# Kernel optimization log

Hardware: AMD Instinct MI355X
Metric: run time of the kernel (lower is better)

## Reference

```python
import jax, jax.numpy as jnp
import numpy as np

N_PER_DEG = 30000
MAX_DEG = 6
MIN_DEG = 0
N_ATOMS = N_PER_DEG * (MAX_DEG + 1)  # 210000, atoms sorted by degree
N_FEAT = 128
NB_FILTER = 128
NB_AFFINE = 2 * MAX_DEG + (1 - MIN_DEG)  # 13


def setup_inputs() -> dict:
    key = jax.random.key(0)
    ks = jax.random.split(key, 2 + MAX_DEG)
    atoms = jax.random.normal(ks[0], (N_ATOMS, N_FEAT), dtype=jnp.float32)
    # glorot-ish scale for the 13 affine weights
    W = jax.random.normal(ks[1], (NB_AFFINE, N_FEAT, NB_FILTER), dtype=jnp.float32) * (1.0 / np.sqrt(N_FEAT))
    b = jnp.zeros((NB_AFFINE, NB_FILTER), dtype=jnp.float32)
    # deg_slice[d] = (start, count) for degree d in 0..MAX_DEG; equal-size buckets
    deg_slice = jnp.asarray(
        np.stack([np.arange(MAX_DEG + 1) * N_PER_DEG,
                  np.full(MAX_DEG + 1, N_PER_DEG)], axis=1).astype(np.int32))
    inp = {"atoms": atoms, "W": W, "b": b, "deg_slice": deg_slice}
    for d in range(1, MAX_DEG + 1):
        inp[f"adj{d}"] = jax.random.randint(ks[1 + d], (N_PER_DEG, d), 0, N_ATOMS, dtype=jnp.int32)
    return inp


def reference(atoms, W, b, deg_slice, adj1, adj2, adj3, adj4, adj5, adj6):
    """Degree-bucketed graph convolution (deepchem GraphConv, linear activation).

    W ordering matches the original iterator: for deg=1..MAX_DEG the pair
    (rel=W[2*(deg-1)], self=W[2*(deg-1)+1]), then deg-0 self uses W[2*MAX_DEG].
    Output concat order: deg 0 bucket first, then deg 1..MAX_DEG.
    """
    adjs = [adj1, adj2, adj3, adj4, adj5, adj6]
    ds = np.asarray(deg_slice)  # structural constant: static slice bounds
    outs = [None] * (MAX_DEG + 1 - MIN_DEG)
    # deg 0: self-affine only
    s0, c0 = int(ds[0, 0]), int(ds[0, 1])
    outs[0] = atoms[s0:s0 + c0] @ W[2 * MAX_DEG] + b[2 * MAX_DEG]
    for deg in range(1, MAX_DEG + 1):
        s, c = int(ds[deg, 0]), int(ds[deg, 1])
        # gather neighbors of each degree-deg atom and sum: (c, deg, F) -> (c, F)
        rel = jnp.take(atoms, adjs[deg - 1], axis=0).sum(axis=1)
        out = (rel @ W[2 * (deg - 1)] + b[2 * (deg - 1)]
               + atoms[s:s + c] @ W[2 * (deg - 1) + 1] + b[2 * (deg - 1) + 1])
        outs[deg] = out
    return jnp.concatenate(outs, axis=0)  # (N_ATOMS, NB_FILTER)
```

## Files before the change

### kernel.cpp

```cpp
#include <hip/hip_runtime.h>
#include <hip/hip_bf16.h>

#define NPD 30000
#define NF  128
#define MAXDEG 6
#define TM  64
#define LDK 136

typedef __attribute__((ext_vector_type(8))) short short8;
typedef __attribute__((ext_vector_type(4))) float floatx4;

__device__ __forceinline__ unsigned short f2bf(float f) {
    __hip_bfloat16 h = __float2bfloat16(f);
    return __builtin_bit_cast(unsigned short, h);
}

__global__ void wt_kernel(const float* __restrict__ W,
                          unsigned short* __restrict__ Wt) {
    __shared__ unsigned short t[32][33];
    const int a  = blockIdx.z;
    const int k0 = blockIdx.x * 32, n0 = blockIdx.y * 32;
    const int tx = threadIdx.x & 31, ty = threadIdx.x >> 5;
    const float*    Wp  = W  + (size_t)a * NF * NF;
    unsigned short* Wtp = Wt + (size_t)a * NF * NF;
#pragma unroll
    for (int i = 0; i < 32; i += 8)
        t[ty + i][tx] = f2bf(Wp[(size_t)(k0 + ty + i) * NF + (n0 + tx)]);
    __syncthreads();
#pragma unroll
    for (int i = 0; i < 32; i += 8)
        Wtp[(size_t)(n0 + ty + i) * NF + (k0 + tx)] = t[tx][ty + i];
}

template <int DEG>
__device__ __forceinline__ void gather_sum(const int* __restrict__ adj,
                                           const float* __restrict__ atoms,
                                           int row_glob, int kc, float* a32) {
    const int* arow = adj + (size_t)row_glob * DEG;
    int idxs[DEG];
#pragma unroll
    for (int j = 0; j < DEG; j++) idxs[j] = arow[j];
#pragma unroll
    for (int i = 0; i < 32; i++) a32[i] = 0.f;
#pragma unroll
    for (int j = 0; j < DEG; j++) {
        const float4* p = (const float4*)(atoms + (size_t)idxs[j] * NF + kc);
#pragma unroll
        for (int q = 0; q < 8; q++) {
            float4 v = p[q];
            a32[q * 4 + 0] += v.x; a32[q * 4 + 1] += v.y;
            a32[q * 4 + 2] += v.z; a32[q * 4 + 3] += v.w;
        }
    }
}

__global__ __launch_bounds__(256) void gconv_kernel(
    const float* __restrict__ atoms,
    const float* __restrict__ W,
    const unsigned short* __restrict__ Wt,
    const float* __restrict__ bvec,
    const int* __restrict__ adj1, const int* __restrict__ adj2,
    const int* __restrict__ adj3, const int* __restrict__ adj4,
    const int* __restrict__ adj5, const int* __restrict__ adj6,
    const int use_wt,
    float* __restrict__ out)
{
    __shared__ unsigned short sA[TM * LDK];

    const int tid  = threadIdx.x;
    const int lane = tid & 63;
    const int wave = tid >> 6;
    const int wr   = wave >> 1, wc = wave & 1;
    const int deg  = blockIdx.y;
    const int row0_local = blockIdx.x * TM;
    const int valid = min(TM, NPD - row0_local);
    const int row0g = deg * NPD + row0_local;

    floatx4 acc[2][4];
#pragma unroll
    for (int i = 0; i < 2; i++)
#pragma unroll
        for (int j = 0; j < 4; j++) acc[i][j] = (floatx4){0.f, 0.f, 0.f, 0.f};

    const int nb = lane & 15;
    const int kq = (lane >> 4) * 8;

    auto run_phase = [&](int wi) {
        const unsigned short* Wtp = Wt + (size_t)wi * NF * NF;
        const float*          Wfp = W  + (size_t)wi * NF * NF;
#pragma unroll
        for (int kk = 0; kk < 4; ++kk) {
            short8 bfr[4];
            if (use_wt) {
#pragma unroll
                for (int nt = 0; nt < 4; ++nt)
                    bfr[nt] = *(const short8*)(Wtp + (size_t)(wc * 64 + nt * 16 + nb) * NF
                                               + kk * 32 + kq);
            } else {
#pragma unroll
                for (int nt = 0; nt < 4; ++nt) {
                    short8 f;
#pragma unroll
                    for (int j = 0; j < 8; ++j)
                        f[j] = (short)f2bf(Wfp[(size_t)(kk * 32 + kq + j) * NF
                                               + (wc * 64 + nt * 16 + nb)]);
                    bfr[nt] = f;
                }
            }
            short8 af[2];
#pragma unroll
            for (int mt = 0; mt < 2; ++mt)
                af[mt] = *(const short8*)(&sA[(wr * 32 + mt * 16 + nb) * LDK + kk * 32 + kq]);
#pragma unroll
            for (int mt = 0; mt < 2; ++mt)
#pragma unroll
                for (int nt = 0; nt < 4; ++nt)
                    acc[mt][nt] = __builtin_amdgcn_mfma_f32_16x16x32_bf16(
                        af[mt], bfr[nt], acc[mt][nt], 0, 0, 0);
        }
    };

    const int rS  = tid >> 2;
    const int kcS = (tid & 3) << 5;
    const int rrS = min(rS, valid - 1);

    {
        const float4* p = (const float4*)(atoms + (size_t)(row0g + rrS) * NF + kcS);
        unsigned ww[16];
#pragma unroll
        for (int q = 0; q < 8; q++) {
            float4 v = p[q];
            ww[q * 2 + 0] = (unsigned)f2bf(v.x) | ((unsigned)f2bf(v.y) << 16);
            ww[q * 2 + 1] = (unsigned)f2bf(v.z) | ((unsigned)f2bf(v.w) << 16);
        }
#pragma unroll
        for (int s = 0; s < 4; s++)
            *(uint4*)(&sA[rS * LDK + kcS + s * 8]) = *(uint4*)&ww[s * 4];
    }
    const int wi_self = (deg == 0) ? 12 : (2 * deg - 1);
    __syncthreads();
    run_phase(wi_self);

    if (deg > 0) {
        __syncthreads();
        float a32[32];
        const int rg = row0_local + rrS;
        switch (deg) {
            case 1: gather_sum<1>(adj1, atoms, rg, kcS, a32); break;
            case 2: gather_sum<2>(adj2, atoms, rg, kcS, a32); break;
            case 3: gather_sum<3>(adj3, atoms, rg, kcS, a32); break;
            case 4: gather_sum<4>(adj4, atoms, rg, kcS, a32); break;
            case 5: gather_sum<5>(adj5, atoms, rg, kcS, a32); break;
            default: gather_sum<6>(adj6, atoms, rg, kcS, a32); break;
        }
        unsigned ww[16];
#pragma unroll
        for (int i = 0; i < 16; i++)
            ww[i] = (unsigned)f2bf(a32[2 * i]) | ((unsigned)f2bf(a32[2 * i + 1]) << 16);
#pragma unroll
        for (int s = 0; s < 4; s++)
            *(uint4*)(&sA[rS * LDK + kcS + s * 8]) = *(uint4*)&ww[s * 4];
        __syncthreads();
        run_phase(2 * (deg - 1));
    }

    float bias[4];
#pragma unroll
    for (int nt = 0; nt < 4; nt++) {
        int n = wc * 64 + nt * 16 + nb;
        float bv = bvec[wi_self * NF + n];
        if (deg > 0) bv += bvec[(2 * (deg - 1)) * NF + n];
        bias[nt] = bv;
    }
    const int rq = (lane >> 4) << 2;
#pragma unroll
    for (int mt = 0; mt < 2; mt++) {
        int rb = wr * 32 + mt * 16 + rq;
#pragma unroll
        for (int reg = 0; reg < 4; reg++) {
            int r = rb + reg;
            if (r < valid) {
                float* op = out + (size_t)(row0g + r) * NF;
#pragma unroll
                for (int nt = 0; nt < 4; nt++) {
                    int n = wc * 64 + nt * 16 + nb;
                    op[n] = acc[mt][nt][reg] + bias[nt];
                }
            }
        }
    }
}

extern "C" void kernel_launch(void* const* d_in, const int* in_sizes, int n_in,
                              void* d_out, int out_size, void* d_ws, size_t ws_size,
                              hipStream_t stream) {
    const float* atoms = (const float*)d_in[0];
    const float* W     = (const float*)d_in[1];
    const float* b     = (const float*)d_in[2];
    const int* adj1 = (const int*)d_in[4];
    const int* adj2 = (const int*)d_in[5];
    const int* adj3 = (const int*)d_in[6];
    const int* adj4 = (const int*)d_in[7];
    const int* adj5 = (const int*)d_in[8];
    const int* adj6 = (const int*)d_in[9];

    const size_t wt_bytes = (size_t)13 * NF * NF * sizeof(unsigned short);
    const int use_wt = (ws_size >= wt_bytes) ? 1 : 0;
    unsigned short* Wt = (unsigned short*)d_ws;

    if (use_wt)
        wt_kernel<<<dim3(4, 4, 13), 256, 0, stream>>>(W, Wt);
    gconv_kernel<<<dim3((NPD + TM - 1) / TM, MAXDEG + 1), 256, 0, stream>>>(
        atoms, W, Wt, b, adj1, adj2, adj3, adj4, adj5, adj6, use_wt,
        (float*)d_out);
}
```

Baseline: 291.8 us.

## Drop LDS staging; each wave loads A fragments directly and owns 32 columns

```diff
diff --git a/kernel.cpp b/kernel.cpp
--- a/kernel.cpp
+++ b/kernel.cpp
@@ -5,7 +5,6 @@
 #define NF  128
 #define MAXDEG 6
 #define TM  64
-#define LDK 136
 
 typedef __attribute__((ext_vector_type(8))) short short8;
 typedef __attribute__((ext_vector_type(4))) float floatx4;
@@ -13,6 +12,14 @@
 __device__ __forceinline__ unsigned short f2bf(float f) {
     __hip_bfloat16 h = __float2bfloat16(f);
     return __builtin_bit_cast(unsigned short, h);
+}
+__device__ __forceinline__ short8 pack8(float4 a, float4 b) {
+    short8 r;
+    r[0] = (short)f2bf(a.x); r[1] = (short)f2bf(a.y);
+    r[2] = (short)f2bf(a.z); r[3] = (short)f2bf(a.w);
+    r[4] = (short)f2bf(b.x); r[5] = (short)f2bf(b.y);
+    r[6] = (short)f2bf(b.z); r[7] = (short)f2bf(b.w);
+    return r;
 }
 
 __global__ void wt_kernel(const float* __restrict__ W,
@@ -32,162 +39,148 @@
         Wtp[(size_t)(n0 + ty + i) * NF + (k0 + tx)] = t[tx][ty + i];
 }
 
+__device__ __forceinline__ void load_bfrags(short8 b[4][2],
+                                            const float* __restrict__ Wf,
+                                            const unsigned short* __restrict__ Wt,
+                                            int use_wt, int wi, int col0, int nb, int kq) {
+    if (use_wt) {
+        const unsigned short* Wp = Wt + (size_t)wi * NF * NF;
+#pragma unroll
+        for (int kk = 0; kk < 4; ++kk)
+#pragma unroll
+            for (int nt = 0; nt < 2; ++nt)
+                b[kk][nt] = *(const short8*)(Wp + (size_t)(col0 + nt * 16 + nb) * NF
+                                             + kk * 32 + kq);
+    } else {
+        const float* Wp = Wf + (size_t)wi * NF * NF;
+#pragma unroll
+        for (int kk = 0; kk < 4; ++kk)
+#pragma unroll
+            for (int nt = 0; nt < 2; ++nt) {
+                short8 f;
+#pragma unroll
+                for (int j = 0; j < 8; ++j)
+                    f[j] = (short)f2bf(Wp[(size_t)(kk * 32 + kq + j) * NF
+                                          + (col0 + nt * 16 + nb)]);
+                b[kk][nt] = f;
+            }
+    }
+}
+
 template <int DEG>
-__device__ __forceinline__ void gather_sum(const int* __restrict__ adj,
-                                           const float* __restrict__ atoms,
-                                           int row_glob, int kc, float* a32) {
-    const int* arow = adj + (size_t)row_glob * DEG;
-    int idxs[DEG];
-#pragma unroll
-    for (int j = 0; j < DEG; j++) idxs[j] = arow[j];
-#pragma unroll
-    for (int i = 0; i < 32; i++) a32[i] = 0.f;
-#pragma unroll
-    for (int j = 0; j < DEG; j++) {
-        const float4* p = (const float4*)(atoms + (size_t)idxs[j] * NF + kc);
-#pragma unroll
-        for (int q = 0; q < 8; q++) {
-            float4 v = p[q];
-            a32[q * 4 + 0] += v.x; a32[q * 4 + 1] += v.y;
-            a32[q * 4 + 2] += v.z; a32[q * 4 + 3] += v.w;
+__device__ __forceinline__ void wave_work(
+    const float* __restrict__ atoms, const float* __restrict__ W,
+    const unsigned short* __restrict__ Wt, const float* __restrict__ bvec,
+    const int* __restrict__ adj, int use_wt,
+    float* __restrict__ out, int row0, int lane, int wave)
+{
+    const int nb   = lane & 15;
+    const int kq   = (lane >> 4) * 8;
+    const int col0 = wave * 32;
+    const int wi_self = (DEG == 0) ? 12 : (2 * DEG - 1);
+    const int wi_rel  = (DEG > 0) ? 2 * (DEG - 1) : 0;
+
+    floatx4 acc[4][2];
+#pragma unroll
+    for (int i = 0; i < 4; i++)
+#pragma unroll
+        for (int j = 0; j < 2; j++) acc[i][j] = (floatx4){0.f, 0.f, 0.f, 0.f};
+
+    {
+        short8 bS[4][2];
+        load_bfrags(bS, W, Wt, use_wt, wi_self, col0, nb, kq);
+#pragma unroll
+        for (int mt = 0; mt < 4; ++mt) {
+            const int rl = min(row0 + mt * 16 + nb, NPD - 1);
+            const float* row = atoms + (size_t)(DEG * NPD + rl) * NF;
+#pragma unroll
+            for (int kk = 0; kk < 4; ++kk) {
+                const float4* p = (const float4*)(row + kk * 32 + kq);
+                float4 v0 = p[0], v1 = p[1];
+                short8 a = pack8(v0, v1);
+#pragma unroll
+                for (int nt = 0; nt < 2; ++nt)
+                    acc[mt][nt] = __builtin_amdgcn_mfma_f32_16x16x32_bf16(
+                        a, bS[kk][nt], acc[mt][nt], 0, 0, 0);
+            }
         }
     }
+
+    if constexpr (DEG > 0) {
+        short8 bR[4][2];
+        load_bfrags(bR, W, Wt, use_wt, wi_rel, col0, nb, kq);
+#pragma unroll
+        for (int mt = 0; mt < 4; ++mt) {
+            const int rl = min(row0 + mt * 16 + nb, NPD - 1);
+            const int* ar = adj + (size_t)rl * DEG;
+            int idxs[DEG];
+#pragma unroll
+            for (int j = 0; j < DEG; ++j) idxs[j] = ar[j];
+#pragma unroll
+            for (int kk = 0; kk < 4; ++kk) {
+                float s[8] = {0.f, 0.f, 0.f, 0.f, 0.f, 0.f, 0.f, 0.f};
+#pragma unroll
+                for (int j = 0; j < DEG; ++j) {
+                    const float4* p = (const float4*)(atoms + (size_t)idxs[j] * NF
+                                                      + kk * 32 + kq);
+                    float4 v0 = p[0], v1 = p[1];
+                    s[0] += v0.x; s[1] += v0.y; s[2] += v0.z; s[3] += v0.w;
+                    s[4] += v1.x; s[5] += v1.y; s[6] += v1.z; s[7] += v1.w;
+                }
+                short8 a;
+#pragma unroll
+                for (int i = 0; i < 8; ++i) a[i] = (short)f2bf(s[i]);
+#pragma unroll
+                for (int nt = 0; nt < 2; ++nt)
+                    acc[mt][nt] = __builtin_amdgcn_mfma_f32_16x16x32_bf16(
+                        a, bR[kk][nt], acc[mt][nt], 0, 0, 0);
+            }
+        }
+    }
+
+    float bias[2];
+#pragma unroll
+    for (int nt = 0; nt < 2; ++nt) {
+        const int n = col0 + nt * 16 + nb;
+        float bv = bvec[wi_self * NF + n];
+        if (DEG > 0) bv += bvec[wi_rel * NF + n];
+        bias[nt] = bv;
+    }
+    const int rq = (lane >> 4) * 4;
+#pragma unroll
+    for (int mt = 0; mt < 4; ++mt) {
+#pragma unroll
+        for (int reg = 0; reg < 4; ++reg) {
+            const int r = row0 + mt * 16 + rq + reg;
+            if (r < NPD) {
+                float* op = out + (size_t)(DEG * NPD + r) * NF;
+#pragma unroll
+                for (int nt = 0; nt < 2; ++nt)
+                    op[col0 + nt * 16 + nb] = acc[mt][nt][reg] + bias[nt];
+            }
+        }
+    }
 }
 
 __global__ __launch_bounds__(256) void gconv_kernel(
-    const float* __restrict__ atoms,
-    const float* __restrict__ W,
-    const unsigned short* __restrict__ Wt,
-    const float* __restrict__ bvec,
+    const float* __restrict__ atoms, const float* __restrict__ W,
+    const unsigned short* __restrict__ Wt, const float* __restrict__ bvec,
     const int* __restrict__ adj1, const int* __restrict__ adj2,
     const int* __restrict__ adj3, const int* __restrict__ adj4,
     const int* __restrict__ adj5, const int* __restrict__ adj6,
-    const int use_wt,
-    float* __restrict__ out)
+    const int use_wt, float* __restrict__ out)
 {
-    __shared__ unsigned short sA[TM * LDK];
-
-    const int tid  = threadIdx.x;
-    const int lane = tid & 63;
-    const int wave = tid >> 6;
-    const int wr   = wave >> 1, wc = wave & 1;
-    const int deg  = blockIdx.y;
-    const int row0_local = blockIdx.x * TM;
-    const int valid = min(TM, NPD - row0_local);
-    const int row0g = deg * NPD + row0_local;
-
-    floatx4 acc[2][4];
-#pragma unroll
-    for (int i = 0; i < 2; i++)
-#pragma unroll
-        for (int j = 0; j < 4; j++) acc[i][j] = (floatx4){0.f, 0.f, 0.f, 0.f};
-
-    const int nb = lane & 15;
-    const int kq = (lane >> 4) * 8;
-
-    auto run_phase = [&](int wi) {
-        const unsigned short* Wtp = Wt + (size_t)wi * NF * NF;
-        const float*          Wfp = W  + (size_t)wi * NF * NF;
-#pragma unroll
-        for (int kk = 0; kk < 4; ++kk) {
-            short8 bfr[4];
-            if (use_wt) {
-#pragma unroll
-                for (int nt = 0; nt < 4; ++nt)
-                    bfr[nt] = *(const short8*)(Wtp + (size_t)(wc * 64 + nt * 16 + nb) * NF
-                                               + kk * 32 + kq);
-            } else {
-#pragma unroll
-                for (int nt = 0; nt < 4; ++nt) {
-                    short8 f;
-#pragma unroll
-                    for (int j = 0; j < 8; ++j)
-                        f[j] = (short)f2bf(Wfp[(size_t)(kk * 32 + kq + j) * NF
-                                               + (wc * 64 + nt * 16 + nb)]);
-                    bfr[nt] = f;
-                }
-            }
-            short8 af[2];
-#pragma unroll
-            for (int mt = 0; mt < 2; ++mt)
-                af[mt] = *(const short8*)(&sA[(wr * 32 + mt * 16 + nb) * LDK + kk * 32 + kq]);
-#pragma unroll
-            for (int mt = 0; mt < 2; ++mt)
-#pragma unroll
-                for (int nt = 0; nt < 4; ++nt)
-                    acc[mt][nt] = __builtin_amdgcn_mfma_f32_16x16x32_bf16(
-                        af[mt], bfr[nt], acc[mt][nt], 0, 0, 0);
-        }
-    };
-
-    const int rS  = tid >> 2;
-    const int kcS = (tid & 3) << 5;
-    const int rrS = min(rS, valid - 1);
-
-    {
-        const float4* p = (const float4*)(atoms + (size_t)(row0g + rrS) * NF + kcS);
-        unsigned ww[16];
-#pragma unroll
-        for (int q = 0; q < 8; q++) {
-            float4 v = p[q];
-            ww[q * 2 + 0] = (unsigned)f2bf(v.x) | ((unsigned)f2bf(v.y) << 16);
-            ww[q * 2 + 1] = (unsigned)f2bf(v.z) | ((unsigned)f2bf(v.w) << 16);
-        }
-#pragma unroll
-        for (int s = 0; s < 4; s++)
-            *(uint4*)(&sA[rS * LDK + kcS + s * 8]) = *(uint4*)&ww[s * 4];
-    }
-    const int wi_self = (deg == 0) ? 12 : (2 * deg - 1);
-    __syncthreads();
-    run_phase(wi_self);
-
-    if (deg > 0) {
-        __syncthreads();
-        float a32[32];
-        const int rg = row0_local + rrS;
-        switch (deg) {
-            case 1: gather_sum<1>(adj1, atoms, rg, kcS, a32); break;
-            case 2: gather_sum<2>(adj2, atoms, rg, kcS, a32); break;
-            case 3: gather_sum<3>(adj3, atoms, rg, kcS, a32); break;
-            case 4: gather_sum<4>(adj4, atoms, rg, kcS, a32); break;
-            case 5: gather_sum<5>(adj5, atoms, rg, kcS, a32); break;
-            default: gather_sum<6>(adj6, atoms, rg, kcS, a32); break;
-        }
-        unsigned ww[16];
-#pragma unroll
-        for (int i = 0; i < 16; i++)
-            ww[i] = (unsigned)f2bf(a32[2 * i]) | ((unsigned)f2bf(a32[2 * i + 1]) << 16);
-#pragma unroll
-        for (int s = 0; s < 4; s++)
-            *(uint4*)(&sA[rS * LDK + kcS + s * 8]) = *(uint4*)&ww[s * 4];
-        __syncthreads();
-        run_phase(2 * (deg - 1));
-    }
-
-    float bias[4];
-#pragma unroll
-    for (int nt = 0; nt < 4; nt++) {
-        int n = wc * 64 + nt * 16 + nb;
-        float bv = bvec[wi_self * NF + n];
-        if (deg > 0) bv += bvec[(2 * (deg - 1)) * NF + n];
-        bias[nt] = bv;
-    }
-    const int rq = (lane >> 4) << 2;
-#pragma unroll
-    for (int mt = 0; mt < 2; mt++) {
-        int rb = wr * 32 + mt * 16 + rq;
-#pragma unroll
-        for (int reg = 0; reg < 4; reg++) {
-            int r = rb + reg;
-            if (r < valid) {
-                float* op = out + (size_t)(row0g + r) * NF;
-#pragma unroll
-                for (int nt = 0; nt < 4; nt++) {
-                    int n = wc * 64 + nt * 16 + nb;
-                    op[n] = acc[mt][nt][reg] + bias[nt];
-                }
-            }
-        }
+    const int lane = threadIdx.x & 63;
+    const int wave = threadIdx.x >> 6;
+    const int row0 = blockIdx.x * TM;
+    switch (blockIdx.y) {
+        case 0: wave_work<0>(atoms, W, Wt, bvec, nullptr, use_wt, out, row0, lane, wave); break;
+        case 1: wave_work<1>(atoms, W, Wt, bvec, adj1,    use_wt, out, row0, lane, wave); break;
+        case 2: wave_work<2>(atoms, W, Wt, bvec, adj2,    use_wt, out, row0, lane, wave); break;
+        case 3: wave_work<3>(atoms, W, Wt, bvec, adj3,    use_wt, out, row0, lane, wave); break;
+        case 4: wave_work<4>(atoms, W, Wt, bvec, adj4,    use_wt, out, row0, lane, wave); break;
+        case 5: wave_work<5>(atoms, W, Wt, bvec, adj5,    use_wt, out, row0, lane, wave); break;
+        default: wave_work<6>(atoms, W, Wt, bvec, adj6,   use_wt, out, row0, lane, wave); break;
     }
 }
 
```

After: 411.6 us. +41.1%, slower.

## Pre-convert atoms to bf16 so the neighbor gather reads half the bytes

Applied to the files above, without the earlier changes.

```diff
diff --git a/kernel.cpp b/kernel.cpp
--- a/kernel.cpp
+++ b/kernel.cpp
@@ -13,6 +13,23 @@
 __device__ __forceinline__ unsigned short f2bf(float f) {
     __hip_bfloat16 h = __float2bfloat16(f);
     return __builtin_bit_cast(unsigned short, h);
+}
+__device__ __forceinline__ float bf2f(unsigned short u) {
+    unsigned v = ((unsigned)u) << 16; return __builtin_bit_cast(float, v);
+}
+__device__ __forceinline__ uint4 pack16B(float4 a, float4 b) {
+    uint4 v;
+    v.x = (unsigned)f2bf(a.x) | ((unsigned)f2bf(a.y) << 16);
+    v.y = (unsigned)f2bf(a.z) | ((unsigned)f2bf(a.w) << 16);
+    v.z = (unsigned)f2bf(b.x) | ((unsigned)f2bf(b.y) << 16);
+    v.w = (unsigned)f2bf(b.z) | ((unsigned)f2bf(b.w) << 16);
+    return v;
+}
+__device__ __forceinline__ void addu4(float* s, uint4 h) {
+    s[0] += bf2f((unsigned short)h.x); s[1] += bf2f((unsigned short)(h.x >> 16));
+    s[2] += bf2f((unsigned short)h.y); s[3] += bf2f((unsigned short)(h.y >> 16));
+    s[4] += bf2f((unsigned short)h.z); s[5] += bf2f((unsigned short)(h.z >> 16));
+    s[6] += bf2f((unsigned short)h.w); s[7] += bf2f((unsigned short)(h.w >> 16));
 }
 
 __global__ void wt_kernel(const float* __restrict__ W,
@@ -32,162 +49,193 @@
         Wtp[(size_t)(n0 + ty + i) * NF + (k0 + tx)] = t[tx][ty + i];
 }
 
-template <int DEG>
-__device__ __forceinline__ void gather_sum(const int* __restrict__ adj,
-                                           const float* __restrict__ atoms,
-                                           int row_glob, int kc, float* a32) {
-    const int* arow = adj + (size_t)row_glob * DEG;
-    int idxs[DEG];
-#pragma unroll
-    for (int j = 0; j < DEG; j++) idxs[j] = arow[j];
-#pragma unroll
-    for (int i = 0; i < 32; i++) a32[i] = 0.f;
-#pragma unroll
-    for (int j = 0; j < DEG; j++) {
-        const float4* p = (const float4*)(atoms + (size_t)idxs[j] * NF + kc);
-#pragma unroll
-        for (int q = 0; q < 8; q++) {
-            float4 v = p[q];
-            a32[q * 4 + 0] += v.x; a32[q * 4 + 1] += v.y;
-            a32[q * 4 + 2] += v.z; a32[q * 4 + 3] += v.w;
-        }
-    }
-}
-
+__global__ __launch_bounds__(256) void cvt_kernel(const float* __restrict__ src,
+                                                  unsigned short* __restrict__ dst) {
+    const size_t i = (size_t)blockIdx.x * 256 + threadIdx.x;
+    const size_t n8 = (size_t)NPD * (MAXDEG + 1) * NF / 8;
+    if (i < n8) {
+        const float4* p = (const float4*)(src + i * 8);
+        ((uint4*)dst)[i] = pack16B(p[0], p[1]);
+    }
+}
+
+__device__ __forceinline__ void load_bfr(short8 b[4], const float* __restrict__ Wf,
+                                         const unsigned short* __restrict__ Wt,
+                                         int use_wt, int wi, int kk,
+                                         int col0, int nb, int kq) {
+    if (use_wt) {
+        const unsigned short* Wp = Wt + (size_t)wi * NF * NF;
+#pragma unroll
+        for (int nt = 0; nt < 4; ++nt)
+            b[nt] = *(const short8*)(Wp + (size_t)(col0 + nt * 16 + nb) * NF + kk * 32 + kq);
+    } else {
+        const float* Wp = Wf + (size_t)wi * NF * NF;
+#pragma unroll
+        for (int nt = 0; nt < 4; ++nt) {
+            short8 f;
+#pragma unroll
+            for (int j = 0; j < 8; ++j)
+                f[j] = (short)f2bf(Wp[(size_t)(kk * 32 + kq + j) * NF + col0 + nt * 16 + nb]);
+            b[nt] = f;
+        }
+    }
+}
+
+template <int DEG, bool BF16A>
+__device__ __forceinline__ void degree_work(
+    const float* __restrict__ atomsF, const unsigned short* __restrict__ atomsH,
+    const float* __restrict__ W, const unsigned short* __restrict__ Wt,
+    const float* __restrict__ bvec, const int* __restrict__ adj,
+    int use_wt, float* __restrict__ out,
+    unsigned short* sA, int* sIdx)
+{
+    const int tid  = threadIdx.x;
+    const int lane = tid & 63, wave = tid >> 6;
+    const int wr = wave >> 1, wc = wave & 1;
+    const int row0_local = blockIdx.x * TM;
+    const int valid = min(TM, NPD - row0_local);
+    const int row0g = DEG * NPD + row0_local;
+    const int nb = lane & 15;
+    const int kq = (lane >> 4) * 8;
+    const int col0 = wc * 64;
+    const int wi_self = (DEG == 0) ? 12 : (2 * DEG - 1);
+    const int wi_rel  = (DEG > 0) ? 2 * (DEG - 1) : 0;
+
+    floatx4 acc[2][4];
+#pragma unroll
+    for (int i = 0; i < 2; i++)
+#pragma unroll
+        for (int j = 0; j < 4; j++) acc[i][j] = (floatx4){0.f, 0.f, 0.f, 0.f};
+
+    if (DEG > 0) {
+        for (int i = tid; i < valid * DEG; i += 256)
+            sIdx[i] = adj[(size_t)row0_local * DEG + i];
+    }
+
+#pragma unroll
+    for (int p = 0; p < 4; ++p) {
+        int idx = p * 256 + tid;
+        int r = idx >> 4, ch = (idx & 15) * 8;
+        int rr = min(r, valid - 1);
+        uint4 v;
+        if (BF16A) {
+            v = *(const uint4*)(atomsH + (size_t)(row0g + rr) * NF + ch);
+        } else {
+            const float4* pf = (const float4*)(atomsF + (size_t)(row0g + rr) * NF + ch);
+            v = pack16B(pf[0], pf[1]);
+        }
+        *(uint4*)&sA[r * LDK + ch] = v;
+    }
+    __syncthreads();
+
+    auto run_phase = [&](int wi) {
+#pragma unroll
+        for (int kk = 0; kk < 4; ++kk) {
+            short8 bfr[4];
+            load_bfr(bfr, W, Wt, use_wt, wi, kk, col0, nb, kq);
+            short8 af[2];
+#pragma unroll
+            for (int mt = 0; mt < 2; ++mt)
+                af[mt] = *(const short8*)&sA[(wr * 32 + mt * 16 + nb) * LDK + kk * 32 + kq];
+#pragma unroll
+            for (int mt = 0; mt < 2; ++mt)
+#pragma unroll
+                for (int nt = 0; nt < 4; ++nt)
+                    acc[mt][nt] = __builtin_amdgcn_mfma_f32_16x16x32_bf16(
+                        af[mt], bfr[nt], acc[mt][nt], 0, 0, 0);
+        }
+    };
+
+    run_phase(wi_self);
+
+    if constexpr (DEG > 0) {
+        __syncthreads();
+#pragma unroll
+        for (int p = 0; p < 2; ++p) {
+            int idx = p * 256 + tid;
+            int r = idx >> 3, kc = (idx & 7) * 16;
+            int rr = min(r, valid - 1);
+            int idxs[DEG];
+#pragma unroll
+            for (int j = 0; j < DEG; ++j) idxs[j] = sIdx[rr * DEG + j];
+            float s[16];
+#pragma unroll
+            for (int i = 0; i < 16; ++i) s[i] = 0.f;
+#pragma unroll
+            for (int j = 0; j < DEG; ++j) {
+                if (BF16A) {
+                    const uint4* ph = (const uint4*)(atomsH + (size_t)idxs[j] * NF + kc);
+                    uint4 h0 = ph[0], h1 = ph[1];
+                    addu4(s, h0); addu4(s + 8, h1);
+                } else {
+                    const float4* pf = (const float4*)(atomsF + (size_t)idxs[j] * NF + kc);
+                    float4 q0 = pf[0], q1 = pf[1], q2 = pf[2], q3 = pf[3];
+                    s[0]  += q0.x; s[1]  += q0.y; s[2]  += q0.z; s[3]  += q0.w;
+                    s[4]  += q1.x; s[5]  += q1.y; s[6]  += q1.z; s[7]  += q1.w;
+                    s[8]  += q2.x; s[9]  += q2.y; s[10] += q2.z; s[11] += q2.w;
+                    s[12] += q3.x; s[13] += q3.y; s[14] += q3.z; s[15] += q3.w;
+                }
+            }
+            uint4 w0, w1;
+            w0.x = (unsigned)f2bf(s[0])  | ((unsigned)f2bf(s[1])  << 16);
+            w0.y = (unsigned)f2bf(s[2])  | ((unsigned)f2bf(s[3])  << 16);
+            w0.z = (unsigned)f2bf(s[4])  | ((unsigned)f2bf(s[5])  << 16);
+            w0.w = (unsigned)f2bf(s[6])  | ((unsigned)f2bf(s[7])  << 16);
+            w1.x = (unsigned)f2bf(s[8])  | ((unsigned)f2bf(s[9])  << 16);
+            w1.y = (unsigned)f2bf(s[10]) | ((unsigned)f2bf(s[11]) << 16);
+            w1.z = (unsigned)f2bf(s[12]) | ((unsigned)f2bf(s[13]) << 16);
+            w1.w = (unsigned)f2bf(s[14]) | ((unsigned)f2bf(s[15]) << 16);
+            *(uint4*)&sA[r * LDK + kc]     = w0;
+            *(uint4*)&sA[r * LDK + kc + 8] = w1;
+        }
+        __syncthreads();
+        run_phase(wi_rel);
+    }
+
+    float bias[4];
+#pragma unroll
+    for (int nt = 0; nt < 4; ++nt) {
+        const int n = col0 + nt * 16 + nb;
+        float bv = bvec[wi_self * NF + n];
+        if (DEG > 0) bv += bvec[wi_rel * NF + n];
+        bias[nt] = bv;
+    }
+    const int rq = (lane >> 4) * 4;
+#pragma unroll
+    for (int mt = 0; mt < 2; ++mt) {
+#pragma unroll
+        for (int reg = 0; reg < 4; ++reg) {
+            const int r = wr * 32 + mt * 16 + rq + reg;
+            if (r < valid) {
+                float* op = out + (size_t)(row0g + r) * NF;
+#pragma unroll
+                for (int nt = 0; nt < 4; ++nt)
+                    op[col0 + nt * 16 + nb] = acc[mt][nt][reg] + bias[nt];
+            }
+        }
+    }
+}
+
+template <bool BF16A>
 __global__ __launch_bounds__(256) void gconv_kernel(
-    const float* __restrict__ atoms,
-    const float* __restrict__ W,
-    const unsigned short* __restrict__ Wt,
+    const float* __restrict__ atomsF, const unsigned short* __restrict__ atomsH,
+    const float* __restrict__ W, const unsigned short* __restrict__ Wt,
     const float* __restrict__ bvec,
     const int* __restrict__ adj1, const int* __restrict__ adj2,
     const int* __restrict__ adj3, const int* __restrict__ adj4,
     const int* __restrict__ adj5, const int* __restrict__ adj6,
-    const int use_wt,
-    float* __restrict__ out)
+    const int use_wt, float* __restrict__ out)
 {
     __shared__ unsigned short sA[TM * LDK];
-
-    const int tid  = threadIdx.x;
-    const int lane = tid & 63;
-    const int wave = tid >> 6;
-    const int wr   = wave >> 1, wc = wave & 1;
-    const int deg  = blockIdx.y;
-    const int row0_local = blockIdx.x * TM;
-    const int valid = min(TM, NPD - row0_local);
-    const int row0g = deg * NPD + row0_local;
-
-    floatx4 acc[2][4];
-#pragma unroll
-    for (int i = 0; i < 2; i++)
-#pragma unroll
-        for (int j = 0; j < 4; j++) acc[i][j] = (floatx4){0.f, 0.f, 0.f, 0.f};
-
-    const int nb = lane & 15;
-    const int kq = (lane >> 4) * 8;
-
-    auto run_phase = [&](int wi) {
-        const unsigned short* Wtp = Wt + (size_t)wi * NF * NF;
-        const float*          Wfp = W  + (size_t)wi * NF * NF;
-#pragma unroll
-        for (int kk = 0; kk < 4; ++kk) {
-            short8 bfr[4];
-            if (use_wt) {
-#pragma unroll
-                for (int nt = 0; nt < 4; ++nt)
-                    bfr[nt] = *(const short8*)(Wtp + (size_t)(wc * 64 + nt * 16 + nb) * NF
-                                               + kk * 32 + kq);
-            } else {
-#pragma unroll
-                for (int nt = 0; nt < 4; ++nt) {
-                    short8 f;
-#pragma unroll
-                    for (int j = 0; j < 8; ++j)
-                        f[j] = (short)f2bf(Wfp[(size_t)(kk * 32 + kq + j) * NF
-                                               + (wc * 64 + nt * 16 + nb)]);
-                    bfr[nt] = f;
-                }
-            }
-            short8 af[2];
-#pragma unroll
-            for (int mt = 0; mt < 2; ++mt)
-                af[mt] = *(const short8*)(&sA[(wr * 32 + mt * 16 + nb) * LDK + kk * 32 + kq]);
-#pragma unroll
-            for (int mt = 0; mt < 2; ++mt)
-#pragma unroll
-                for (int nt = 0; nt < 4; ++nt)
-                    acc[mt][nt] = __builtin_amdgcn_mfma_f32_16x16x32_bf16(
-                        af[mt], bfr[nt], acc[mt][nt], 0, 0, 0);
-        }
-    };
-
-    const int rS  = tid >> 2;
-    const int kcS = (tid & 3) << 5;
-    const int rrS = min(rS, valid - 1);
-
-    {
-        const float4* p = (const float4*)(atoms + (size_t)(row0g + rrS) * NF + kcS);
-        unsigned ww[16];
-#pragma unroll
-        for (int q = 0; q < 8; q++) {
-            float4 v = p[q];
-            ww[q * 2 + 0] = (unsigned)f2bf(v.x) | ((unsigned)f2bf(v.y) << 16);
-            ww[q * 2 + 1] = (unsigned)f2bf(v.z) | ((unsigned)f2bf(v.w) << 16);
-        }
-#pragma unroll
-        for (int s = 0; s < 4; s++)
-            *(uint4*)(&sA[rS * LDK + kcS + s * 8]) = *(uint4*)&ww[s * 4];
-    }
-    const int wi_self = (deg == 0) ? 12 : (2 * deg - 1);
-    __syncthreads();
-    run_phase(wi_self);
-
-    if (deg > 0) {
-        __syncthreads();
-        float a32[32];
-        const int rg = row0_local + rrS;
-        switch (deg) {
-            case 1: gather_sum<1>(adj1, atoms, rg, kcS, a32); break;
-            case 2: gather_sum<2>(adj2, atoms, rg, kcS, a32); break;
-            case 3: gather_sum<3>(adj3, atoms, rg, kcS, a32); break;
-            case 4: gather_sum<4>(adj4, atoms, rg, kcS, a32); break;
-            case 5: gather_sum<5>(adj5, atoms, rg, kcS, a32); break;
-            default: gather_sum<6>(adj6, atoms, rg, kcS, a32); break;
-        }
-        unsigned ww[16];
-#pragma unroll
-        for (int i = 0; i < 16; i++)
-            ww[i] = (unsigned)f2bf(a32[2 * i]) | ((unsigned)f2bf(a32[2 * i + 1]) << 16);
-#pragma unroll
-        for (int s = 0; s < 4; s++)
-            *(uint4*)(&sA[rS * LDK + kcS + s * 8]) = *(uint4*)&ww[s * 4];
-        __syncthreads();
-        run_phase(2 * (deg - 1));
-    }
-
-    float bias[4];
-#pragma unroll
-    for (int nt = 0; nt < 4; nt++) {
-        int n = wc * 64 + nt * 16 + nb;
-        float bv = bvec[wi_self * NF + n];
-        if (deg > 0) bv += bvec[(2 * (deg - 1)) * NF + n];
-        bias[nt] = bv;
-    }
-    const int rq = (lane >> 4) << 2;
-#pragma unroll
-    for (int mt = 0; mt < 2; mt++) {
-        int rb = wr * 32 + mt * 16 + rq;
-#pragma unroll
-        for (int reg = 0; reg < 4; reg++) {
-            int r = rb + reg;
-            if (r < valid) {
-                float* op = out + (size_t)(row0g + r) * NF;
-#pragma unroll
-                for (int nt = 0; nt < 4; nt++) {
-                    int n = wc * 64 + nt * 16 + nb;
-                    op[n] = acc[mt][nt][reg] + bias[nt];
-                }
-            }
-        }
+    __shared__ int sIdx[TM * MAXDEG];
+    switch (blockIdx.y) {
+        case 0: degree_work<0, BF16A>(atomsF, atomsH, W, Wt, bvec, nullptr, use_wt, out, sA, sIdx); break;
+        case 1: degree_work<1, BF16A>(atomsF, atomsH, W, Wt, bvec, adj1,    use_wt, out, sA, sIdx); break;
+        case 2: degree_work<2, BF16A>(atomsF, atomsH, W, Wt, bvec, adj2,    use_wt, out, sA, sIdx); break;
+        case 3: degree_work<3, BF16A>(atomsF, atomsH, W, Wt, bvec, adj3,    use_wt, out, sA, sIdx); break;
+        case 4: degree_work<4, BF16A>(atomsF, atomsH, W, Wt, bvec, adj4,    use_wt, out, sA, sIdx); break;
+        case 5: degree_work<5, BF16A>(atomsF, atomsH, W, Wt, bvec, adj5,    use_wt, out, sA, sIdx); break;
+        default: degree_work<6, BF16A>(atomsF, atomsH, W, Wt, bvec, adj6,   use_wt, out, sA, sIdx); break;
     }
 }
 
@@ -205,12 +253,23 @@
     const int* adj6 = (const int*)d_in[9];
 
     const size_t wt_bytes = (size_t)13 * NF * NF * sizeof(unsigned short);
-    const int use_wt = (ws_size >= wt_bytes) ? 1 : 0;
-    unsigned short* Wt = (unsigned short*)d_ws;
+    const size_t at_bytes = (size_t)NPD * (MAXDEG + 1) * NF * sizeof(unsigned short);
+    const int use_wt   = (ws_size >= wt_bytes) ? 1 : 0;
+    const int use_bf16 = (ws_size >= wt_bytes + at_bytes) ? 1 : 0;
+    unsigned short* Wt     = (unsigned short*)d_ws;
+    unsigned short* atomsH = (unsigned short*)((char*)d_ws + wt_bytes);
 
     if (use_wt)
         wt_kernel<<<dim3(4, 4, 13), 256, 0, stream>>>(W, Wt);
-    gconv_kernel<<<dim3((NPD + TM - 1) / TM, MAXDEG + 1), 256, 0, stream>>>(
-        atoms, W, Wt, b, adj1, adj2, adj3, adj4, adj5, adj6, use_wt,
-        (float*)d_out);
-}
+    if (use_bf16) {
+        const int n8 = NPD * (MAXDEG + 1) * NF / 8;
+        cvt_kernel<<<(n8 + 255) / 256, 256, 0, stream>>>(atoms, atomsH);
+        gconv_kernel<true><<<dim3((NPD + TM - 1) / TM, MAXDEG + 1), 256, 0, stream>>>(
+            atoms, atomsH, W, Wt, b, adj1, adj2, adj3, adj4, adj5, adj6, use_wt,
+            (float*)d_out);
+    } else {
+        gconv_kernel<false><<<dim3((NPD + TM - 1) / TM, MAXDEG + 1), 256, 0, stream>>>(
+            atoms, atomsH, W, Wt, b, adj1, adj2, adj3, adj4, adj5, adj6, use_wt,
+            (float*)d_out);
+    }
+}
```

Result: faster. 274.8 us (-5.8%).
